# Kernel tuning notes

Measured on AMD Instinct MI355X. Metric: run time of the kernel, lower is better.

The kernel has to match this reference:

```python
import jax, jax.numpy as jnp
import numpy as np

ALPHA = 0.001
TAU = 1.0
KAPPA = 1.0
N_ITER = 1


def setup_inputs() -> dict:
    key = jax.random.key(0)
    k1, k2, k3, k4, k5 = jax.random.split(key, 5)
    B, H, N, K = 8, 8, 512, 16
    mu = jax.random.normal(k1, (B, N, K), dtype=jnp.float32)
    # beta: softmax-like attention weights over j (positive, rows sum to 1)
    beta = jax.nn.softmax(jax.random.normal(k2, (B, H, N, N), dtype=jnp.float32), axis=-1)
    mu_prior = jax.random.normal(k3, (B, N, K), dtype=jnp.float32)
    phi = 0.1 * jax.random.normal(k4, (B, N, 3), dtype=jnp.float32)
    g = jax.random.normal(k5, (3, K, K), dtype=jnp.float32)
    generators = 0.5 * (g - jnp.swapaxes(g, -1, -2))  # skew-symmetric so(3) rep -> stable expm
    lr = jnp.asarray(0.05, dtype=jnp.float32)
    return {"mu": mu, "beta": beta, "mu_prior": mu_prior, "phi": phi,
            "generators": generators, "lr": lr}


def _transport(mu, phi, generators):
    # phi_algebra[b,n] = sum_g phi[b,n,g] * G_g  -> (B,N,K,K)
    B, N, K = mu.shape
    phi_alg = jnp.einsum('bng,gkl->bnkl', phi, generators)
    expm = jax.vmap(jax.scipy.linalg.expm)
    Om_i = expm(phi_alg.reshape(B * N, K, K)).reshape(B, N, K, K)
    Om_j_inv = expm((-phi_alg).reshape(B * N, K, K)).reshape(B, N, K, K)
    # mu_t[b,i,j] = Om_i[b,i] @ (Om_j_inv[b,j] @ mu[b,j])  (factored, avoids (B,N,N,K,K))
    v = jnp.einsum('bjlm,bjm->bjl', Om_j_inv, mu)          # (B,N,K)
    mu_t = jnp.einsum('bikl,bjl->bijk', Om_i, v)           # (B,N,N,K)
    return mu_t


def reference(mu, beta, mu_prior, phi, generators, lr):
    beta_avg = beta.mean(axis=1)                           # (B,N,N)
    mu_cur = mu
    for _ in range(N_ITER):
        grad_prior = ALPHA * (mu_cur - mu_prior)
        mu_t = _transport(mu_cur, phi, generators)         # (B,N,N,K)
        delta = mu_cur[:, :, None, :] - mu_t               # (B,N,N,K)
        # TERM 1: sum_j (beta_ij/tau) * delta_ij
        grad1 = jnp.einsum('bij,bijk->bik', beta_avg, delta) / TAU
        # TERM 2 (second-order): sum_j sum_k (beta_ij/kappa)(delta_jk - beta_ik) KL_ij gkl_ik
        #   = (1/kappa)[ sum_j beta_ij KL_ij gkl_ij - (sum_j beta_ij KL_ij) * sum_k beta_ik gkl_ik ]
        kl = jnp.sum(delta * delta, axis=-1) / (2.0 * TAU)  # (B,N,N)
        gkl = delta / TAU                                   # (B,N,N,K)
        w = beta_avg * kl                                   # (B,N,N)
        term1 = jnp.einsum('bij,bijk->bik', w, gkl)
        s = jnp.sum(w, axis=-1)                             # (B,N)
        bsum = jnp.einsum('bij,bijk->bik', beta_avg, gkl)
        grad2 = (term1 - s[..., None] * bsum) / KAPPA
        mu_cur = mu_cur - lr * (grad_prior + grad1 + grad2)
    return mu_cur
```

## Files before the change

### kernel.cpp

```cpp
#include <hip/hip_runtime.h>
#include <hip/hip_bf16.h>
#include <cstddef>
#include <cstdint>

#define B_ 8
#define H_ 8
#define N_ 512
#define K_ 16
#define NN_ (N_*N_)

static constexpr float ALPHA_C = 0.001f;

typedef float f32x4 __attribute__((ext_vector_type(4)));

#define LDSTRIDE 20

__device__ __forceinline__ void mm_rowB(const float* a, const float* Bbuf,
                                        int c0, f32x4& acc)
{
    #pragma unroll
    for (int k = 0; k < 16; ++k) {
        const f32x4 bk = *(const f32x4*)&Bbuf[k * LDSTRIDE + c0];
        acc.x = fmaf(a[k], bk.x, acc.x);
        acc.y = fmaf(a[k], bk.y, acc.y);
        acc.z = fmaf(a[k], bk.z, acc.z);
        acc.w = fmaf(a[k], bk.w, acc.w);
    }
}

__device__ __forceinline__ void read_row(const float* buf, int r, float* a)
{
    #pragma unroll
    for (int i = 0; i < 4; ++i) {
        const f32x4 t = *(const f32x4*)&buf[r * LDSTRIDE + 4 * i];
        a[4*i]   = t.x; a[4*i+1] = t.y; a[4*i+2] = t.z; a[4*i+3] = t.w;
    }
}

__device__ __forceinline__ void write_strip(float* buf, int r, int c0, f32x4 s)
{
    *(f32x4*)&buf[r * LDSTRIDE + c0] = s;
}

__global__ __launch_bounds__(256) void expm_beta_kernel(
    const float* __restrict__ mu, const float* __restrict__ phi,
    const float* __restrict__ gen, const float* __restrict__ beta,
    float* __restrict__ Om, float* __restrict__ v, float* __restrict__ q,
    float* __restrict__ bavg)
{
    __shared__ float lds[4][2][16 * LDSTRIDE];

    const int tid  = threadIdx.x;
    const int w    = tid >> 6, lane = tid & 63;
    const int r    = lane >> 2, c0 = (lane & 3) << 2;
    const int bn   = (blockIdx.x << 2) | w;
    const int bb   = bn >> 9;
    const int nn   = bn & 511;

    float* U0 = lds[w][0];
    float* U1 = lds[w][1];

    const float p0 = phi[bn*3+0], p1 = phi[bn*3+1], p2 = phi[bn*3+2];
    const int gidx = r * 16 + c0;
    const f32x4 g0 = *(const f32x4*)&gen[gidx];
    const f32x4 g1 = *(const f32x4*)&gen[256 + gidx];
    const f32x4 g2 = *(const f32x4*)&gen[512 + gidx];
    const float mur = mu[bn * 16 + r];

    const size_t betaBase = (((size_t)bb * H_) * N_ + nn) * N_;
    const float* bp = beta + betaBase + (lane << 2);
    f32x4 bt[16];
    #pragma unroll
    for (int h = 0; h < H_; ++h) {
        bt[2*h+0] = __builtin_nontemporal_load((const f32x4*)(bp + (size_t)h * NN_));
        bt[2*h+1] = __builtin_nontemporal_load((const f32x4*)(bp + (size_t)h * NN_ + 256));
    }

    f32x4 As;
    As.x = p0*g0.x + p1*g1.x + p2*g2.x;
    As.y = p0*g0.y + p1*g1.y + p2*g2.y;
    As.z = p0*g0.z + p1*g1.z + p2*g2.z;
    As.w = p0*g0.w + p1*g1.w + p2*g2.w;

    float t = As.x*As.x + As.y*As.y + As.z*As.z + As.w*As.w;
    #pragma unroll
    for (int m = 1; m <= 32; m <<= 1) t += __shfl_xor(t, m, 64);
    float theta = sqrtf(t);
    int s = 0;
    while (theta > 2.0f && s < 30) { theta *= 0.5f; ++s; }
    const float sc = exp2f((float)(-s));
    const f32x4 Xs = As * sc;

    write_strip(U0, r, c0, Xs);
    float xrow[16];
    read_row(U0, r, xrow);

    f32x4 a2s = {0.f, 0.f, 0.f, 0.f};
    mm_rowB(xrow, U0, c0, a2s);
    write_strip(U1, r, c0, a2s);

    f32x4 a3s = {0.f, 0.f, 0.f, 0.f};
    mm_rowB(xrow, U1, c0, a3s);

    f32x4 pa0 = (bt[0] + bt[2]) + (bt[4] + bt[6]);
    f32x4 pa1 = (bt[1] + bt[3]) + (bt[5] + bt[7]);

    float a2row[16];
    read_row(U1, r, a2row);
    f32x4 a4s = {0.f, 0.f, 0.f, 0.f};
    mm_rowB(a2row, U1, c0, a4s);
    write_strip(U0, r, c0, a4s);
    float a4row[16];
    read_row(U0, r, a4row);

    f32x4 di = {0.f, 0.f, 0.f, 0.f};
    if (r >= c0 && r < c0 + 4) ((float*)&di)[r - c0] = 1.0f;

    const f32x4 C0 = di + Xs + a2s * 0.5f + a3s * (1.0f/6.0f);
    const f32x4 C1 = di * (1.0f/24.0f) + Xs * (1.0f/120.0f)
                   + a2s * (1.0f/720.0f) + a3s * (1.0f/5040.0f);
    const f32x4 Q2 = di * (1.0f/40320.0f) + Xs * (1.0f/362880.0f)
                   + a2s * (1.0f/3628800.0f) + a3s * (1.0f/39916800.0f)
                   + a4s * (1.0f/479001600.0f);

    write_strip(U1, r, c0, Q2);
    f32x4 T1 = C1;
    mm_rowB(a4row, U1, c0, T1);

    {
        const f32x4 rv0 = (pa0 + ((bt[8]+bt[10]) + (bt[12]+bt[14]))) * 0.125f;
        const f32x4 rv1 = (pa1 + ((bt[9]+bt[11]) + (bt[13]+bt[15]))) * 0.125f;
        float* bo = bavg + (size_t)bn * N_ + (lane << 2);
        *(f32x4*)bo         = rv0;
        *(f32x4*)(bo + 256) = rv1;
    }

    write_strip(U1, r, c0, T1);
    f32x4 P = C0;
    mm_rowB(a4row, U1, c0, P);

    for (int it = 0; it < s; ++it) {
        write_strip(U1, r, c0, P);
        float prow[16];
        read_row(U1, r, prow);
        f32x4 Pn = {0.f, 0.f, 0.f, 0.f};
        mm_rowB(prow, U1, c0, Pn);
        P = Pn;
    }

    *(f32x4*)&Om[(size_t)bn * 256 + r * 16 + c0] = P;

    f32x4 vc = P * mur;
    #pragma unroll
    for (int m = 4; m <= 32; m <<= 1) {
        vc.x += __shfl_xor(vc.x, m, 64);
        vc.y += __shfl_xor(vc.y, m, 64);
        vc.z += __shfl_xor(vc.z, m, 64);
        vc.w += __shfl_xor(vc.w, m, 64);
    }
    if (r == 0) *(f32x4*)&v[bn * 16 + c0] = vc;

    float qp = vc.x*vc.x + vc.y*vc.y + vc.z*vc.z + vc.w*vc.w;
    qp += __shfl_xor(qp, 1, 64);
    qp += __shfl_xor(qp, 2, 64);
    if (lane == 0) q[bn] = 0.5f * qp;
}

__device__ __forceinline__ float fold16(float* wc, int lane)
{
    #pragma unroll
    for (int k = 0; k < 8; ++k) {
        const bool up = (lane & 32) != 0;
        const float send = up ? wc[k] : wc[k + 8];
        const float recv = __shfl_xor(send, 32, 64);
        wc[k] = (up ? wc[k + 8] : wc[k]) + recv;
    }
    #pragma unroll
    for (int k = 0; k < 4; ++k) {
        const bool up = (lane & 16) != 0;
        const float send = up ? wc[k] : wc[k + 4];
        const float recv = __shfl_xor(send, 16, 64);
        wc[k] = (up ? wc[k + 4] : wc[k]) + recv;
    }
    #pragma unroll
    for (int k = 0; k < 2; ++k) {
        const bool up = (lane & 8) != 0;
        const float send = up ? wc[k] : wc[k + 2];
        const float recv = __shfl_xor(send, 8, 64);
        wc[k] = (up ? wc[k + 2] : wc[k]) + recv;
    }
    {
        const bool up = (lane & 4) != 0;
        const float send = up ? wc[0] : wc[1];
        const float recv = __shfl_xor(send, 4, 64);
        wc[0] = (up ? wc[1] : wc[0]) + recv;
    }
    wc[0] += __shfl_xor(wc[0], 2, 64);
    wc[0] += __shfl_xor(wc[0], 1, 64);
    return wc[0];
}

__device__ __forceinline__ float rot_reduce(const float* omr, float gv, int lane)
{
    float pr[4];
    #pragma unroll
    for (int rr = 0; rr < 4; ++rr) pr[rr] = omr[rr] * gv;

    #pragma unroll
    for (int k = 0; k < 2; ++k) {
        const bool up = (lane & 4) != 0;
        const float send = up ? pr[k] : pr[k + 2];
        const float recv = __shfl_xor(send, 4, 64);
        pr[k] = (up ? pr[k + 2] : pr[k]) + recv;
    }
    {
        const bool up = (lane & 8) != 0;
        const float send = up ? pr[0] : pr[1];
        const float recv = __shfl_xor(send, 8, 64);
        pr[0] = (up ? pr[1] : pr[0]) + recv;
    }
    pr[0] += __shfl_xor(pr[0], 16, 64);
    pr[0] += __shfl_xor(pr[0], 32, 64);
    return pr[0];
}

__global__ __launch_bounds__(256, 2) void grad_kernel(
    const float* __restrict__ mu, const float* __restrict__ mu_prior,
    const float* __restrict__ lrp, const float* __restrict__ Om,
    const float* __restrict__ v, const float* __restrict__ q,
    const float* __restrict__ bavg, float* __restrict__ out)
{
    __shared__ float v_t[16 * 516];
    __shared__ f32x4 q4[128];

    const int blk = blockIdx.x;
    const int b   = blk >> 6;
    const int i0  = (blk & 63) << 3;
    const int tid = threadIdx.x;
    const int wid = tid >> 6, lane = tid & 63;
    const int ia  = i0 + wid;
    const int ib  = i0 + 4 + wid;
    const size_t rowia = (size_t)b * N_ + ia;
    const size_t rowib = (size_t)b * N_ + ib;

    const float* vb = v + (size_t)b * N_ * K_;
    f32x4 tq[8];
    #pragma unroll
    for (int s = 0; s < 8; ++s)
        tq[s] = *(const f32x4*)&vb[(tid + 256 * s) << 2];

    f32x4 qreg = {0.f, 0.f, 0.f, 0.f};
    const f32x4* qb4 = (const f32x4*)(q + (size_t)b * N_);
    if (tid < 128) qreg = qb4[tid];

    const float* bpa = bavg + rowia * N_ + (lane << 2);
    const float* bpb = bavg + rowib * N_ + (lane << 2);
    const f32x4 rvA0 = *(const f32x4*)bpa;
    const f32x4 rvA1 = *(const f32x4*)(bpa + 256);
    const f32x4 rvB0 = *(const f32x4*)bpb;
    const f32x4 rvB1 = *(const f32x4*)(bpb + 256);

    #pragma unroll
    for (int s = 0; s < 8; ++s) {
        const int f4 = tid + 256 * s;
        const int j  = f4 >> 2;
        const int k0 = (f4 & 3) << 2;
        v_t[(k0+0) * 516 + j] = tq[s].x;
        v_t[(k0+1) * 516 + j] = tq[s].y;
        v_t[(k0+2) * 516 + j] = tq[s].z;
        v_t[(k0+3) * 516 + j] = tq[s].w;
    }
    if (tid < 128) q4[tid] = qreg;
    __syncthreads();

    float via[16], vib[16];
    #pragma unroll
    for (int k = 0; k < 16; ++k) { via[k] = v_t[k * 516 + ia]; vib[k] = v_t[k * 516 + ib]; }
    const float qia = ((const float*)q4)[ia];
    const float qib = ((const float*)q4)[ib];

    const int j0 = lane << 2;

    float dAa0=0.f,dAa1=0.f,dAa2=0.f,dAa3=0.f, dAb0=0.f,dAb1=0.f,dAb2=0.f,dAb3=0.f;
    #pragma unroll
    for (int k = 0; k < 16; ++k) {
        const f32x4 vj = *(const f32x4*)&v_t[k * 516 + j0];
        dAa0 = fmaf(via[k], vj.x, dAa0);
        dAa1 = fmaf(via[k], vj.y, dAa1);
        dAa2 = fmaf(via[k], vj.z, dAa2);
        dAa3 = fmaf(via[k], vj.w, dAa3);
        dAb0 = fmaf(vib[k], vj.x, dAb0);
        dAb1 = fmaf(vib[k], vj.y, dAb1);
        dAb2 = fmaf(vib[k], vj.z, dAb2);
        dAb3 = fmaf(vib[k], vj.w, dAb3);
    }
    float dBa0=0.f,dBa1=0.f,dBa2=0.f,dBa3=0.f, dBb0=0.f,dBb1=0.f,dBb2=0.f,dBb3=0.f;
    #pragma unroll
    for (int k = 0; k < 16; ++k) {
        const f32x4 vj = *(const f32x4*)&v_t[k * 516 + j0 + 256];
        dBa0 = fmaf(via[k], vj.x, dBa0);
        dBa1 = fmaf(via[k], vj.y, dBa1);
        dBa2 = fmaf(via[k], vj.z, dBa2);
        dBa3 = fmaf(via[k], vj.w, dBa3);
        dBb0 = fmaf(vib[k], vj.x, dBb0);
        dBb1 = fmaf(vib[k], vj.y, dBb1);
        dBb2 = fmaf(vib[k], vj.z, dBb2);
        dBb3 = fmaf(vib[k], vj.w, dBb3);
    }

    const f32x4 qjA = q4[lane];
    const f32x4 qjB = q4[lane | 64];

    const float rklAa0 = rvA0.x * (qia + qjA.x - dAa0);
    const float rklAa1 = rvA0.y * (qia + qjA.y - dAa1);
    const float rklAa2 = rvA0.z * (qia + qjA.z - dAa2);
    const float rklAa3 = rvA0.w * (qia + qjA.w - dAa3);
    const float rklBa0 = rvA1.x * (qia + qjB.x - dBa0);
    const float rklBa1 = rvA1.y * (qia + qjB.y - dBa1);
    const float rklBa2 = rvA1.z * (qia + qjB.z - dBa2);
    const float rklBa3 = rvA1.w * (qia + qjB.w - dBa3);

    const float rklAb0 = rvB0.x * (qib + qjA.x - dAb0);
    const float rklAb1 = rvB0.y * (qib + qjA.y - dAb1);
    const float rklAb2 = rvB0.z * (qib + qjA.z - dAb2);
    const float rklAb3 = rvB0.w * (qib + qjA.w - dAb3);
    const float rklBb0 = rvB1.x * (qib + qjB.x - dBb0);
    const float rklBb1 = rvB1.y * (qib + qjB.y - dBb1);
    const float rklBb2 = rvB1.z * (qib + qjB.z - dBb2);
    const float rklBb3 = rvB1.w * (qib + qjB.w - dBb3);

    float sacc_a = ((rklAa0 + rklAa1) + (rklAa2 + rklAa3))
                 + ((rklBa0 + rklBa1) + (rklBa2 + rklBa3));
    float sacc_b = ((rklAb0 + rklAb1) + (rklAb2 + rklAb3))
                 + ((rklBb0 + rklBb1) + (rklBb2 + rklBb3));
    float R_a = ((rvA0.x + rvA0.y) + (rvA0.z + rvA0.w))
              + ((rvA1.x + rvA1.y) + (rvA1.z + rvA1.w));
    float R_b = ((rvB0.x + rvB0.y) + (rvB0.z + rvB0.w))
              + ((rvB1.x + rvB1.y) + (rvB1.z + rvB1.w));

    const int cmine = (lane >> 2) & 15;
    const int tqi   = lane & 3;
    const float* omba = Om + rowia * 256;
    const float* ombb = Om + rowib * 256;
    float omra[4], omrb[4];
    #pragma unroll
    for (int rr = 0; rr < 4; ++rr) {
        omra[rr] = omba[(4 * tqi + rr) * 16 + cmine];
        omrb[rr] = ombb[(4 * tqi + rr) * 16 + cmine];
    }
    const int row = 4 * tqi + 2 * ((lane >> 2) & 1) + ((lane >> 3) & 1);
    const size_t oia = rowia * 16 + row;
    const size_t oib = rowib * 16 + row;
    float m0a = 0.f, mpa = 0.f, m0b = 0.f, mpb = 0.f;
    if (lane < 16) {
        m0a = mu[oia]; mpa = mu_prior[oia];
        m0b = mu[oib]; mpb = mu_prior[oib];
    }
    const float lrv = lrp[0];

    #pragma unroll
    for (int off = 32; off > 0; off >>= 1) {
        sacc_a += __shfl_xor(sacc_a, off, 64);
        R_a    += __shfl_xor(R_a,    off, 64);
        sacc_b += __shfl_xor(sacc_b, off, 64);
        R_b    += __shfl_xor(R_b,    off, 64);
    }
    const float oms_a  = 1.0f - sacc_a;
    const float coef_a = oms_a * R_a + sacc_a;
    const float oms_b  = 1.0f - sacc_b;
    const float coef_b = oms_b * R_b + sacc_b;

    const float cAa0 = fmaf(oms_a, rvA0.x, rklAa0);
    const float cAa1 = fmaf(oms_a, rvA0.y, rklAa1);
    const float cAa2 = fmaf(oms_a, rvA0.z, rklAa2);
    const float cAa3 = fmaf(oms_a, rvA0.w, rklAa3);
    const float cBa0 = fmaf(oms_a, rvA1.x, rklBa0);
    const float cBa1 = fmaf(oms_a, rvA1.y, rklBa1);
    const float cBa2 = fmaf(oms_a, rvA1.z, rklBa2);
    const float cBa3 = fmaf(oms_a, rvA1.w, rklBa3);
    const float cAb0 = fmaf(oms_b, rvB0.x, rklAb0);
    const float cAb1 = fmaf(oms_b, rvB0.y, rklAb1);
    const float cAb2 = fmaf(oms_b, rvB0.z, rklAb2);
    const float cAb3 = fmaf(oms_b, rvB0.w, rklAb3);
    const float cBb0 = fmaf(oms_b, rvB1.x, rklBb0);
    const float cBb1 = fmaf(oms_b, rvB1.y, rklBb1);
    const float cBb2 = fmaf(oms_b, rvB1.z, rklBb2);
    const float cBb3 = fmaf(oms_b, rvB1.w, rklBb3);

    float wca[16], wcb[16];
    #pragma unroll
    for (int k = 0; k < 16; ++k) { wca[k] = 0.f; wcb[k] = 0.f; }

    #pragma unroll
    for (int k = 0; k < 16; ++k) {
        const f32x4 vj = *(const f32x4*)&v_t[k * 516 + j0];
        float t1 = fmaf(cAa0, vj.x, wca[k]);
        t1 = fmaf(cAa1, vj.y, t1);
        t1 = fmaf(cAa2, vj.z, t1);
        wca[k] = fmaf(cAa3, vj.w, t1);
        float t2 = fmaf(cAb0, vj.x, wcb[k]);
        t2 = fmaf(cAb1, vj.y, t2);
        t2 = fmaf(cAb2, vj.z, t2);
        wcb[k] = fmaf(cAb3, vj.w, t2);
    }
    #pragma unroll
    for (int k = 0; k < 16; ++k) {
        const f32x4 vj = *(const f32x4*)&v_t[k * 516 + j0 + 256];
        float t1 = fmaf(cBa0, vj.x, wca[k]);
        t1 = fmaf(cBa1, vj.y, t1);
        t1 = fmaf(cBa2, vj.z, t1);
        wca[k] = fmaf(cBa3, vj.w, t1);
        float t2 = fmaf(cBb0, vj.x, wcb[k]);
        t2 = fmaf(cBb1, vj.y, t2);
        t2 = fmaf(cBb2, vj.z, t2);
        wcb[k] = fmaf(cBb3, vj.w, t2);
    }

    const float wfa = fold16(wca, lane);
    const float wfb = fold16(wcb, lane);

    const float gva = coef_a * v_t[cmine * 516 + ia] - wfa;
    const float gvb = coef_b * v_t[cmine * 516 + ib] - wfb;
    const float pra = rot_reduce(omra, gva, lane);
    const float prb = rot_reduce(omrb, gvb, lane);

    if (lane < 16) {
        out[oia] = m0a - lrv * (ALPHA_C * (m0a - mpa) + pra);
        out[oib] = m0b - lrv * (ALPHA_C * (m0b - mpb) + prb);
    }
}

extern "C" void kernel_launch(void* const* d_in, const int* in_sizes, int n_in,
                              void* d_out, int out_size, void* d_ws, size_t ws_size,
                              hipStream_t stream)
{
    const float* mu   = (const float*)d_in[0];
    const float* beta = (const float*)d_in[1];
    const float* mup  = (const float*)d_in[2];
    const float* phi  = (const float*)d_in[3];
    const float* gen  = (const float*)d_in[4];
    const float* lr   = (const float*)d_in[5];
    float* out = (float*)d_out;

    float* Om   = (float*)d_ws;
    float* v    = Om + (size_t)4096 * 256;
    float* q    = v  + (size_t)4096 * 16;
    float* bavg = q  + (size_t)4096;

    expm_beta_kernel<<<B_ * N_ / 4, 256, 0, stream>>>(mu, phi, gen, beta, Om, v, q, bavg);
    grad_kernel<<<B_ * (N_ / 8), 256, 0, stream>>>(mu, mup, lr, Om, v, q, bavg, out);
}
```

Measured before the change: 117.4 us.

## Split beta head-averaging between expm kernel and grad kernel

```diff
diff --git a/kernel.cpp b/kernel.cpp
--- a/kernel.cpp
+++ b/kernel.cpp
@@ -69,9 +69,9 @@
 
     const size_t betaBase = (((size_t)bb * H_) * N_ + nn) * N_;
     const float* bp = beta + betaBase + (lane << 2);
-    f32x4 bt[16];
-    #pragma unroll
-    for (int h = 0; h < H_; ++h) {
+    f32x4 bt[8];
+    #pragma unroll
+    for (int h = 0; h < 4; ++h) {
         bt[2*h+0] = __builtin_nontemporal_load((const f32x4*)(bp + (size_t)h * NN_));
         bt[2*h+1] = __builtin_nontemporal_load((const f32x4*)(bp + (size_t)h * NN_ + 256));
     }
@@ -102,8 +102,13 @@
     f32x4 a3s = {0.f, 0.f, 0.f, 0.f};
     mm_rowB(xrow, U1, c0, a3s);
 
-    f32x4 pa0 = (bt[0] + bt[2]) + (bt[4] + bt[6]);
-    f32x4 pa1 = (bt[1] + bt[3]) + (bt[5] + bt[7]);
+    {
+        const f32x4 s0 = (bt[0] + bt[2]) + (bt[4] + bt[6]);
+        const f32x4 s1 = (bt[1] + bt[3]) + (bt[5] + bt[7]);
+        float* bo = bavg + (size_t)bn * N_ + (lane << 2);
+        *(f32x4*)bo         = s0;
+        *(f32x4*)(bo + 256) = s1;
+    }
 
     float a2row[16];
     read_row(U1, r, a2row);
@@ -127,14 +132,6 @@
     f32x4 T1 = C1;
     mm_rowB(a4row, U1, c0, T1);
 
-    {
-        const f32x4 rv0 = (pa0 + ((bt[8]+bt[10]) + (bt[12]+bt[14]))) * 0.125f;
-        const f32x4 rv1 = (pa1 + ((bt[9]+bt[11]) + (bt[13]+bt[15]))) * 0.125f;
-        float* bo = bavg + (size_t)bn * N_ + (lane << 2);
-        *(f32x4*)bo         = rv0;
-        *(f32x4*)(bo + 256) = rv1;
-    }
-
     write_strip(U1, r, c0, T1);
     f32x4 P = C0;
     mm_rowB(a4row, U1, c0, P);
@@ -225,10 +222,11 @@
 }
 
 __global__ __launch_bounds__(256, 2) void grad_kernel(
-    const float* __restrict__ mu, const float* __restrict__ mu_prior,
-    const float* __restrict__ lrp, const float* __restrict__ Om,
-    const float* __restrict__ v, const float* __restrict__ q,
-    const float* __restrict__ bavg, float* __restrict__ out)
+    const float* __restrict__ mu, const float* __restrict__ beta,
+    const float* __restrict__ mu_prior, const float* __restrict__ lrp,
+    const float* __restrict__ Om, const float* __restrict__ v,
+    const float* __restrict__ q, const float* __restrict__ bavg,
+    float* __restrict__ out)
 {
     __shared__ float v_t[16 * 516];
     __shared__ f32x4 q4[128];
@@ -253,12 +251,16 @@
     const f32x4* qb4 = (const f32x4*)(q + (size_t)b * N_);
     if (tid < 128) qreg = qb4[tid];
 
-    const float* bpa = bavg + rowia * N_ + (lane << 2);
-    const float* bpb = bavg + rowib * N_ + (lane << 2);
-    const f32x4 rvA0 = *(const f32x4*)bpa;
-    const f32x4 rvA1 = *(const f32x4*)(bpa + 256);
-    const f32x4 rvB0 = *(const f32x4*)bpb;
-    const f32x4 rvB1 = *(const f32x4*)(bpb + 256);
+    const float* bA = beta + ((size_t)b * H_ * N_ + ia) * N_ + (lane << 2);
+    const float* bB = beta + ((size_t)b * H_ * N_ + ib) * N_ + (lane << 2);
+    f32x4 bt[16];
+    #pragma unroll
+    for (int h = 4; h < 8; ++h) {
+        bt[2*(h-4)+0] = __builtin_nontemporal_load((const f32x4*)(bA + (size_t)h * NN_));
+        bt[2*(h-4)+1] = __builtin_nontemporal_load((const f32x4*)(bA + (size_t)h * NN_ + 256));
+        bt[2*(h-4)+8] = __builtin_nontemporal_load((const f32x4*)(bB + (size_t)h * NN_));
+        bt[2*(h-4)+9] = __builtin_nontemporal_load((const f32x4*)(bB + (size_t)h * NN_ + 256));
+    }
 
     #pragma unroll
     for (int s = 0; s < 8; ++s) {
@@ -272,6 +274,18 @@
     }
     if (tid < 128) q4[tid] = qreg;
     __syncthreads();
+
+    const float* bpa = bavg + rowia * N_ + (lane << 2);
+    const float* bpb = bavg + rowib * N_ + (lane << 2);
+    const f32x4 pA0 = *(const f32x4*)bpa;
+    const f32x4 pA1 = *(const f32x4*)(bpa + 256);
+    const f32x4 pB0 = *(const f32x4*)bpb;
+    const f32x4 pB1 = *(const f32x4*)(bpb + 256);
+
+    const f32x4 rvA0 = (pA0 + ((bt[0] + bt[2]) + (bt[4] + bt[6])))  * 0.125f;
+    const f32x4 rvA1 = (pA1 + ((bt[1] + bt[3]) + (bt[5] + bt[7])))  * 0.125f;
+    const f32x4 rvB0 = (pB0 + ((bt[8] + bt[10]) + (bt[12] + bt[14]))) * 0.125f;
+    const f32x4 rvB1 = (pB1 + ((bt[9] + bt[11]) + (bt[13] + bt[15]))) * 0.125f;
 
     float via[16], vib[16];
     #pragma unroll
@@ -448,5 +462,5 @@
     float* bavg = q  + (size_t)4096;
 
     expm_beta_kernel<<<B_ * N_ / 4, 256, 0, stream>>>(mu, phi, gen, beta, Om, v, q, bavg);
-    grad_kernel<<<B_ * (N_ / 8), 256, 0, stream>>>(mu, mup, lr, Om, v, q, bavg, out);
-}
+    grad_kernel<<<B_ * (N_ / 8), 256, 0, stream>>>(mu, beta, mup, lr, Om, v, q, bavg, out);
+}
```

Measured after the change: 126.2 us. +7.5%, slower.
